# Optimization experiments

Measured on AMD Instinct MI355X. Metric: run time of the kernel, lower is better.

The kernel has to match this reference:

```python
import jax, jax.numpy as jnp
import numpy as np

B, C, H, W = 2, 3, 96, 96
D = 32  # qkv channels

def setup_inputs() -> dict:
    key = jax.random.key(0)
    ks = jax.random.split(key, 9)
    s3 = 1.0 / np.sqrt(3.0)
    sD = 1.0 / np.sqrt(float(D))
    return {
        "image": jax.random.normal(ks[0], (B, C, H, W), dtype=jnp.float32),
        "key_w": jax.random.normal(ks[1], (D, C), dtype=jnp.float32) * s3,
        "key_b": jax.random.normal(ks[2], (D,), dtype=jnp.float32) * 0.01,
        "query_w": jax.random.normal(ks[3], (D, C), dtype=jnp.float32) * s3,
        "query_b": jax.random.normal(ks[4], (D,), dtype=jnp.float32) * 0.01,
        "value_w": jax.random.normal(ks[5], (D, C), dtype=jnp.float32) * s3,
        "value_b": jax.random.normal(ks[6], (D,), dtype=jnp.float32) * 0.01,
        "out_w": jax.random.normal(ks[7], (C, D), dtype=jnp.float32) * sD,
        "out_b": jax.random.normal(ks[8], (C,), dtype=jnp.float32) * 0.01,
    }

def reference(image, key_w, key_b, query_w, query_b, value_w, value_b, out_w, out_b):
    b, c, h, w = image.shape
    n = h * w
    x = image.reshape(b, c, n)  # [B,3,N]
    # 1x1 convs == per-pixel linear maps over channels
    f_x = jnp.einsum('dc,bcn->bdn', key_w, x) + key_b[None, :, None]    # key   [B,D,N]
    g_x = jnp.einsum('dc,bcn->bdn', query_w, x) + query_b[None, :, None]  # query [B,D,N]
    h_x = jnp.einsum('dc,bcn->bdn', value_w, x) + value_b[None, :, None]  # value [B,D,N]
    # s = f_x^T @ g_x : [B,N,N]; softmax over dim=1 (first N axis), as in torch code
    s = jnp.einsum('bdn,bdm->bnm', f_x, g_x)
    beta = jax.nn.softmax(s, axis=1)
    # v = h_x @ beta : [B,D,N]
    v = jnp.einsum('bdn,bnm->bdm', h_x, beta)
    # output 1x1 conv D->3, then clamp
    o = jnp.einsum('cd,bdm->bcm', out_w, v) + out_b[None, :, None]
    o = jnp.clip(o, -1.0, 1.0)
    return o.reshape(b, c, h, w)
```

## Files before the change

### kernel.cpp

```cpp
#include <hip/hip_runtime.h>
#include <hip/hip_fp16.h>

#define BB 2
#define CC 3
#define NN 9216
#define DD 32
#define NSPLIT 4
#define KSPLIT 2
#define KEYS_PER_WAVE (NN / (KSPLIT * NSPLIT))
#define CHUNKS (KEYS_PER_WAVE / 64)
#define NGROUP (BB * NN / 32)
#define L2E 1.44269504f
#define SZH ((size_t)BB * NN * DD)

typedef _Float16 half8 __attribute__((ext_vector_type(8)));
typedef _Float16 half4v __attribute__((ext_vector_type(4)));
typedef __fp16 fp16x2 __attribute__((ext_vector_type(2)));
typedef float float4v __attribute__((ext_vector_type(4)));

#define MFMA_K32(a, b, c) __builtin_amdgcn_mfma_f32_16x16x32_f16((a), (b), (c), 0, 0, 0)

__global__ __launch_bounds__(256) void prep_kernel(
    const float* __restrict__ img,
    const float* __restrict__ kw, const float* __restrict__ kb,
    const float* __restrict__ qw, const float* __restrict__ qb,
    const float* __restrict__ vw, const float* __restrict__ vb,
    const float* __restrict__ ow,
    _Float16* __restrict__ fH,
    _Float16* __restrict__ gH, _Float16* __restrict__ gL,
    _Float16* __restrict__ hP)
{
    __shared__ float wsm[256];
    __shared__ float cwb[12];
    int bid = blockIdx.x;
    int t = threadIdx.x;
    if (bid < 288) {
        float v;
        if (t < 96)       v = kw[t];
        else if (t < 192) v = qw[t - 96];
        else if (t < 224) v = kb[t - 192];
        else              v = qb[t - 224];
        wsm[t] = v;
        __syncthreads();

        int id = bid * 256 + t;
        int part = id & 3;
        int n = (id >> 2) % NN;
        int b = (id >> 2) / NN;
        const float* xb = img + (size_t)b * CC * NN + n;
        float x0 = xb[0], x1 = xb[NN], x2 = xb[2 * NN];
        half8 fh, gh, gl;
#pragma unroll
        for (int j = 0; j < 8; j++) {
            int d = part * 8 + j;
            float fv = wsm[d * 3 + 0] * x0 + wsm[d * 3 + 1] * x1 +
                       wsm[d * 3 + 2] * x2 + wsm[192 + d];
            float gv = (wsm[96 + d * 3 + 0] * x0 + wsm[96 + d * 3 + 1] * x1 +
                        wsm[96 + d * 3 + 2] * x2 + wsm[224 + d]) * L2E;
            _Float16 ghi = (_Float16)gv;
            fh[j] = (_Float16)fv;
            gh[j] = ghi; gl[j] = (_Float16)(gv - (float)ghi);
        }
        size_t off = ((size_t)b * NN + n) * DD + part * 8;
        *(half8*)(fH + off) = fh;
        *(half8*)(gH + off) = gh;
        *(half8*)(gL + off) = gl;
    } else {
        if (t < 9) {
            int c = t / 3, k = t % 3;
            float s = 0.f;
#pragma unroll
            for (int d = 0; d < DD; d++) s += ow[c * DD + d] * vw[d * 3 + k];
            cwb[t] = s;
        } else if (t < 12) {
            int c = t - 9;
            float s = 0.f;
#pragma unroll
            for (int d = 0; d < DD; d++) s += ow[c * DD + d] * vb[d];
            cwb[9 + c] = s;
        }
        __syncthreads();
        const int N8 = NN / 8;
        int id = (bid - 288) * 256 + t;
        int n8 = id % N8;
        int row = (id / N8) & 3;
        int b = id / (N8 * 4);
        half8 hv = {1, 1, 1, 1, 1, 1, 1, 1};
        if (row < 3) {
            const float* xb = img + (size_t)b * CC * NN + n8 * 8;
            float w0 = cwb[row * 3 + 0], w1 = cwb[row * 3 + 1],
                  w2 = cwb[row * 3 + 2], bv = cwb[9 + row];
#pragma unroll
            for (int j = 0; j < 8; j++)
                hv[j] = (_Float16)(w0 * xb[j] + w1 * xb[NN + j] + w2 * xb[2 * NN + j] + bv);
        }
        *(half8*)(hP + ((size_t)(b * 4 + row)) * NN + n8 * 8) = hv;
    }
}

__device__ __forceinline__ void softmax_store(float4v (&s)[4], float& mrun,
                                              float4v& acc, _Float16* Pw,
                                              int l16, int quad)
{
    float a0 = fmaxf(fmaxf(s[0][0], s[0][1]), s[0][2]);
    float a1 = fmaxf(fmaxf(s[0][3], s[1][0]), s[1][1]);
    float a2 = fmaxf(fmaxf(s[1][2], s[1][3]), s[2][0]);
    float a3 = fmaxf(fmaxf(s[2][1], s[2][2]), s[2][3]);
    float a4 = fmaxf(fmaxf(s[3][0], s[3][1]), s[3][2]);
    float lmax = fmaxf(fmaxf(fmaxf(a0, a1), fmaxf(a2, a3)), fmaxf(a4, s[3][3]));
    if (__any(lmax > 8.f)) {
        float mx = fmaxf(lmax, __shfl_xor(lmax, 16, 64));
        mx = fmaxf(mx, __shfl_xor(mx, 32, 64));
        float d = fmaxf(mx, 0.f);
        float alpha = __builtin_amdgcn_exp2f(-d);
#pragma unroll
        for (int r = 0; r < 4; r++) acc[r] *= alpha;
        mrun += d;
#pragma unroll
        for (int blk = 0; blk < 4; blk++)
#pragma unroll
            for (int j = 0; j < 4; j++) s[blk][j] -= d;
    }
#pragma unroll
    for (int blk = 0; blk < 4; blk++) {
        float p0 = __builtin_amdgcn_exp2f(s[blk][0]);
        float p1 = __builtin_amdgcn_exp2f(s[blk][1]);
        float p2 = __builtin_amdgcn_exp2f(s[blk][2]);
        float p3 = __builtin_amdgcn_exp2f(s[blk][3]);
        union { fp16x2 h2[2]; half4v h4; } u;
        u.h2[0] = __builtin_amdgcn_cvt_pkrtz(p0, p1);
        u.h2[1] = __builtin_amdgcn_cvt_pkrtz(p2, p3);
        *(half4v*)(Pw + l16 * 72 + blk * 16 + quad * 4) = u.h4;
    }
}

__global__ __launch_bounds__(256)
__attribute__((amdgpu_waves_per_eu(6, 6)))
void attn_partial_kernel(
    const _Float16* __restrict__ ws,
    float* __restrict__ pnum, float* __restrict__ pM)
{
    const _Float16* fH = ws;
    const _Float16* gH = ws + SZH;
    const _Float16* hP = ws + 3 * SZH;

    const int gb = blockIdx.x;
    const int g  = gb / KSPLIT;
    const int ks = gb % KSPLIT;
    const int b = g / (NN / 32);
    const int m0 = (g % (NN / 32)) * 32;
    const int tid = threadIdx.x;
    const int w = tid >> 6;
    const int lane = tid & 63;
    const int l16 = lane & 15;
    const int quad = lane >> 4;

    union SMem {
        _Float16 P[NSPLIT * 2 * 16 * 72];
        struct { float acc[NSPLIT][4][33]; float mbuf[NSPLIT][32]; } mg;
    };
    __shared__ __align__(16) SMem sm;

    const _Float16* gHb = gH + ((size_t)b * NN + m0 + l16) * DD + quad * 8;
    half8 qh0 = *(const half8*)(gHb);
    half8 ql0 = *(const half8*)(gHb + SZH);
    half8 qh1 = *(const half8*)(gHb + (size_t)16 * DD);
    half8 ql1 = *(const half8*)(gHb + SZH + (size_t)16 * DD);

    float4v acc0 = {0,0,0,0};
    float4v acc1 = {0,0,0,0};
    float mrun0 = 0.f;
    float mrun1 = 0.f;

    const int nbase = ks * (NN / KSPLIT) + w * KEYS_PER_WAVE;
    const int vrow = (l16 < 3) ? l16 : 3;
    const _Float16* vp = hP + ((size_t)(b * 4 + vrow)) * NN + nbase + quad * 8;
    const _Float16* kp = fH + ((size_t)b * NN + nbase + l16) * DD + quad * 8;
    _Float16* Pw0 = sm.P + (size_t)(w * 2 + 0) * 16 * 72;
    _Float16* Pw1 = sm.P + (size_t)(w * 2 + 1) * 16 * 72;

    half8 kC[4];
#pragma unroll
    for (int blk = 0; blk < 4; blk++)
        kC[blk] = *(const half8*)(kp + (size_t)(blk * 16) * DD);
    kp += (size_t)64 * DD;

    for (int c = 0; c < CHUNKS; ++c) {
        float4v s[4];
        {
            float4v zm0 = {-mrun0, -mrun0, -mrun0, -mrun0};
#pragma unroll
            for (int blk = 0; blk < 4; blk++) {
                float4v t0 = MFMA_K32(kC[blk], ql0, zm0);
                s[blk] = MFMA_K32(kC[blk], qh0, t0);
            }
        }
        softmax_store(s, mrun0, acc0, Pw0, l16, quad);

        {
            float4v zm1 = {-mrun1, -mrun1, -mrun1, -mrun1};
#pragma unroll
            for (int blk = 0; blk < 4; blk++) {
                float4v t1 = MFMA_K32(kC[blk], ql1, zm1);
                s[blk] = MFMA_K32(kC[blk], qh1, t1);
                kC[blk] = *(const half8*)(kp + (size_t)(blk * 16) * DD);
            }
        }
        kp += (size_t)64 * DD;

        half8 vA0 = *(const half8*)(vp);
        half8 vA1 = *(const half8*)(vp + 32);

        softmax_store(s, mrun1, acc1, Pw1, l16, quad);

        {
            half8 pf0 = *(const half8*)(Pw0 + l16 * 72 + quad * 8);
            half8 pf1 = *(const half8*)(Pw0 + l16 * 72 + 32 + quad * 8);
            acc0 = MFMA_K32(vA0, pf0, acc0);
            acc0 = MFMA_K32(vA1, pf1, acc0);
            half8 qf0 = *(const half8*)(Pw1 + l16 * 72 + quad * 8);
            half8 qf1 = *(const half8*)(Pw1 + l16 * 72 + 32 + quad * 8);
            acc1 = MFMA_K32(vA0, qf0, acc1);
            acc1 = MFMA_K32(vA1, qf1, acc1);
        }
        vp += 64;
    }

    __syncthreads();

    if (quad == 0) {
#pragma unroll
        for (int r = 0; r < 4; r++) {
            sm.mg.acc[w][r][l16]      = acc0[r];
            sm.mg.acc[w][r][l16 + 16] = acc1[r];
        }
        sm.mg.mbuf[w][l16]      = mrun0;
        sm.mg.mbuf[w][l16 + 16] = mrun1;
    }
    __syncthreads();

    if (tid < 4 * 32) {
        int c = tid >> 5, m = tid & 31;
        float M = sm.mg.mbuf[0][m];
#pragma unroll
        for (int s2 = 1; s2 < NSPLIT; s2++) M = fmaxf(M, sm.mg.mbuf[s2][m]);
        float v = 0.f;
#pragma unroll
        for (int s2 = 0; s2 < NSPLIT; s2++)
            v += sm.mg.acc[s2][c][m] * __builtin_amdgcn_exp2f(sm.mg.mbuf[s2][m] - M);
        pnum[(size_t)gb * 128 + tid] = v;
        if (c == 0) pM[gb * 32 + m] = M;
    }
}

__global__ __launch_bounds__(128) void merge_kernel(
    const float* __restrict__ pnum, const float* __restrict__ pM,
    const float* __restrict__ ob, float* __restrict__ out)
{
    const int g = blockIdx.x;
    const int b = g / (NN / 32);
    const int m0 = (g % (NN / 32)) * 32;
    const int tid = threadIdx.x;

    if (tid < CC * 32) {
        int c = tid >> 5, m = tid & 31;
        int base = g * KSPLIT;
        float M = pM[base * 32 + m];
#pragma unroll
        for (int k = 1; k < KSPLIT; k++) M = fmaxf(M, pM[(base + k) * 32 + m]);
        float num = 0.f, L = 0.f;
#pragma unroll
        for (int k = 0; k < KSPLIT; k++) {
            float e = __builtin_amdgcn_exp2f(pM[(base + k) * 32 + m] - M);
            num += pnum[(size_t)(base + k) * 128 + c * 32 + m] * e;
            L   += pnum[(size_t)(base + k) * 128 + 96 + m] * e;
        }
        float o = num / L + ob[c];
        o = fminf(1.f, fmaxf(-1.f, o));
        out[((size_t)b * CC + c) * NN + m0 + m] = o;
    }
}

extern "C" void kernel_launch(void* const* d_in, const int* in_sizes, int n_in,
                              void* d_out, int out_size, void* d_ws, size_t ws_size,
                              hipStream_t stream) {
    const float* img = (const float*)d_in[0];
    const float* kw  = (const float*)d_in[1];
    const float* kb  = (const float*)d_in[2];
    const float* qw  = (const float*)d_in[3];
    const float* qb  = (const float*)d_in[4];
    const float* vw  = (const float*)d_in[5];
    const float* vb  = (const float*)d_in[6];
    const float* ow  = (const float*)d_in[7];
    const float* ob  = (const float*)d_in[8];
    float* out = (float*)d_out;

    _Float16* fH = (_Float16*)d_ws;
    _Float16* gH = fH + SZH;
    _Float16* gL = gH + SZH;
    _Float16* hP = gL + SZH;
    float* pnum = (float*)(hP + (size_t)BB * 4 * NN);
    float* pM   = pnum + (size_t)NGROUP * KSPLIT * 128;

    prep_kernel<<<324, 256, 0, stream>>>(img, kw, kb, qw, qb, vw, vb, ow,
                                         fH, gH, gL, hP);
    attn_partial_kernel<<<NGROUP * KSPLIT, 256, 0, stream>>>(
        (const _Float16*)d_ws, pnum, pM);
    merge_kernel<<<NGROUP, 128, 0, stream>>>(pnum, pM, ob, out);
}
```

Measured before the change: 111.9 us.

## Permute key rows so softmax probabilities feed PV MFMA directly from registers

The prep kernel now stores key rows in a permuted order within each 32-key group, so the QK^T MFMA output layout matches the B-operand layout required by the PV MFMA. The softmax packs the exponentiated scores straight into half8 registers, which removes the LDS store/load round trip for P and the shared P buffer. This cuts LDS traffic and shared memory use per block, in exchange for coupling the key layout to the MFMA register mapping. The value loads are also moved earlier so they can overlap with the softmax.

```diff
diff --git a/kernel.cpp b/kernel.cpp
--- a/kernel.cpp
+++ b/kernel.cpp
@@ -61,8 +61,14 @@
             fh[j] = (_Float16)fv;
             gh[j] = ghi; gl[j] = (_Float16)(gv - (float)ghi);
         }
+        int within = n & 31;
+        int q  = within >> 3;
+        int rm = within & 7;
+        int bh = rm >> 2;
+        int jj = rm & 3;
+        int nperm = (n & ~31) | (bh << 4) | (q << 2) | jj;
+        *(half8*)(fH + ((size_t)b * NN + nperm) * DD + part * 8) = fh;
         size_t off = ((size_t)b * NN + n) * DD + part * 8;
-        *(half8*)(fH + off) = fh;
         *(half8*)(gH + off) = gh;
         *(half8*)(gL + off) = gl;
     } else {
@@ -98,9 +104,8 @@
     }
 }
 
-__device__ __forceinline__ void softmax_store(float4v (&s)[4], float& mrun,
-                                              float4v& acc, _Float16* Pw,
-                                              int l16, int quad)
+__device__ __forceinline__ void softmax_pack(float4v (&s)[4], float& mrun,
+                                             float4v& acc, half8& pa, half8& pb)
 {
     float a0 = fmaxf(fmaxf(s[0][0], s[0][1]), s[0][2]);
     float a1 = fmaxf(fmaxf(s[0][3], s[1][0]), s[1][1]);
@@ -121,17 +126,24 @@
 #pragma unroll
             for (int j = 0; j < 4; j++) s[blk][j] -= d;
     }
-#pragma unroll
-    for (int blk = 0; blk < 4; blk++) {
-        float p0 = __builtin_amdgcn_exp2f(s[blk][0]);
-        float p1 = __builtin_amdgcn_exp2f(s[blk][1]);
-        float p2 = __builtin_amdgcn_exp2f(s[blk][2]);
-        float p3 = __builtin_amdgcn_exp2f(s[blk][3]);
-        union { fp16x2 h2[2]; half4v h4; } u;
-        u.h2[0] = __builtin_amdgcn_cvt_pkrtz(p0, p1);
-        u.h2[1] = __builtin_amdgcn_cvt_pkrtz(p2, p3);
-        *(half4v*)(Pw + l16 * 72 + blk * 16 + quad * 4) = u.h4;
-    }
+    union { fp16x2 h2[4]; half8 h8; } ua, ub;
+    ua.h2[0] = __builtin_amdgcn_cvt_pkrtz(__builtin_amdgcn_exp2f(s[0][0]),
+                                          __builtin_amdgcn_exp2f(s[0][1]));
+    ua.h2[1] = __builtin_amdgcn_cvt_pkrtz(__builtin_amdgcn_exp2f(s[0][2]),
+                                          __builtin_amdgcn_exp2f(s[0][3]));
+    ua.h2[2] = __builtin_amdgcn_cvt_pkrtz(__builtin_amdgcn_exp2f(s[1][0]),
+                                          __builtin_amdgcn_exp2f(s[1][1]));
+    ua.h2[3] = __builtin_amdgcn_cvt_pkrtz(__builtin_amdgcn_exp2f(s[1][2]),
+                                          __builtin_amdgcn_exp2f(s[1][3]));
+    ub.h2[0] = __builtin_amdgcn_cvt_pkrtz(__builtin_amdgcn_exp2f(s[2][0]),
+                                          __builtin_amdgcn_exp2f(s[2][1]));
+    ub.h2[1] = __builtin_amdgcn_cvt_pkrtz(__builtin_amdgcn_exp2f(s[2][2]),
+                                          __builtin_amdgcn_exp2f(s[2][3]));
+    ub.h2[2] = __builtin_amdgcn_cvt_pkrtz(__builtin_amdgcn_exp2f(s[3][0]),
+                                          __builtin_amdgcn_exp2f(s[3][1]));
+    ub.h2[3] = __builtin_amdgcn_cvt_pkrtz(__builtin_amdgcn_exp2f(s[3][2]),
+                                          __builtin_amdgcn_exp2f(s[3][3]));
+    pa = ua.h8; pb = ub.h8;
 }
 
 __global__ __launch_bounds__(256)
@@ -155,11 +167,10 @@
     const int l16 = lane & 15;
     const int quad = lane >> 4;
 
-    union SMem {
-        _Float16 P[NSPLIT * 2 * 16 * 72];
-        struct { float acc[NSPLIT][4][33]; float mbuf[NSPLIT][32]; } mg;
-    };
-    __shared__ __align__(16) SMem sm;
+    __shared__ __align__(16) struct {
+        float acc[NSPLIT][4][33];
+        float mbuf[NSPLIT][32];
+    } sm;
 
     const _Float16* gHb = gH + ((size_t)b * NN + m0 + l16) * DD + quad * 8;
     half8 qh0 = *(const half8*)(gHb);
@@ -176,8 +187,6 @@
     const int vrow = (l16 < 3) ? l16 : 3;
     const _Float16* vp = hP + ((size_t)(b * 4 + vrow)) * NN + nbase + quad * 8;
     const _Float16* kp = fH + ((size_t)b * NN + nbase + l16) * DD + quad * 8;
-    _Float16* Pw0 = sm.P + (size_t)(w * 2 + 0) * 16 * 72;
-    _Float16* Pw1 = sm.P + (size_t)(w * 2 + 1) * 16 * 72;
 
     half8 kC[4];
 #pragma unroll
@@ -187,6 +196,7 @@
 
     for (int c = 0; c < CHUNKS; ++c) {
         float4v s[4];
+        half8 pa0, pb0, pa1, pb1;
         {
             float4v zm0 = {-mrun0, -mrun0, -mrun0, -mrun0};
 #pragma unroll
@@ -195,7 +205,10 @@
                 s[blk] = MFMA_K32(kC[blk], qh0, t0);
             }
         }
-        softmax_store(s, mrun0, acc0, Pw0, l16, quad);
+        half8 vA0 = *(const half8*)(vp);
+        half8 vA1 = *(const half8*)(vp + 32);
+
+        softmax_pack(s, mrun0, acc0, pa0, pb0);
 
         {
             float4v zm1 = {-mrun1, -mrun1, -mrun1, -mrun1};
@@ -208,46 +221,35 @@
         }
         kp += (size_t)64 * DD;
 
-        half8 vA0 = *(const half8*)(vp);
-        half8 vA1 = *(const half8*)(vp + 32);
-
-        softmax_store(s, mrun1, acc1, Pw1, l16, quad);
-
-        {
-            half8 pf0 = *(const half8*)(Pw0 + l16 * 72 + quad * 8);
-            half8 pf1 = *(const half8*)(Pw0 + l16 * 72 + 32 + quad * 8);
-            acc0 = MFMA_K32(vA0, pf0, acc0);
-            acc0 = MFMA_K32(vA1, pf1, acc0);
-            half8 qf0 = *(const half8*)(Pw1 + l16 * 72 + quad * 8);
-            half8 qf1 = *(const half8*)(Pw1 + l16 * 72 + 32 + quad * 8);
-            acc1 = MFMA_K32(vA0, qf0, acc1);
-            acc1 = MFMA_K32(vA1, qf1, acc1);
-        }
+        softmax_pack(s, mrun1, acc1, pa1, pb1);
+
+        acc0 = MFMA_K32(vA0, pa0, acc0);
+        acc0 = MFMA_K32(vA1, pb0, acc0);
+        acc1 = MFMA_K32(vA0, pa1, acc1);
+        acc1 = MFMA_K32(vA1, pb1, acc1);
         vp += 64;
     }
 
-    __syncthreads();
-
     if (quad == 0) {
 #pragma unroll
         for (int r = 0; r < 4; r++) {
-            sm.mg.acc[w][r][l16]      = acc0[r];
-            sm.mg.acc[w][r][l16 + 16] = acc1[r];
-        }
-        sm.mg.mbuf[w][l16]      = mrun0;
-        sm.mg.mbuf[w][l16 + 16] = mrun1;
+            sm.acc[w][r][l16]      = acc0[r];
+            sm.acc[w][r][l16 + 16] = acc1[r];
+        }
+        sm.mbuf[w][l16]      = mrun0;
+        sm.mbuf[w][l16 + 16] = mrun1;
     }
     __syncthreads();
 
     if (tid < 4 * 32) {
         int c = tid >> 5, m = tid & 31;
-        float M = sm.mg.mbuf[0][m];
-#pragma unroll
-        for (int s2 = 1; s2 < NSPLIT; s2++) M = fmaxf(M, sm.mg.mbuf[s2][m]);
+        float M = sm.mbuf[0][m];
+#pragma unroll
+        for (int s2 = 1; s2 < NSPLIT; s2++) M = fmaxf(M, sm.mbuf[s2][m]);
         float v = 0.f;
 #pragma unroll
         for (int s2 = 0; s2 < NSPLIT; s2++)
-            v += sm.mg.acc[s2][c][m] * __builtin_amdgcn_exp2f(sm.mg.mbuf[s2][m] - M);
+            v += sm.acc[s2][c][m] * __builtin_amdgcn_exp2f(sm.mbuf[s2][m] - M);
         pnum[(size_t)gb * 128 + tid] = v;
         if (c == 0) pM[gb * 32 + m] = M;
     }
```

Result: slower. 160.3 us (+43.3%).
